# Optimization experiments

Hardware: AMD Instinct MI355X
Metric: run time of the kernel (lower is better)

The kernel has to match this reference:

```python
import jax, jax.numpy as jnp
import numpy as np


def setup_inputs() -> dict:
    key = jax.random.key(0)
    kx, kd = jax.random.split(key)
    B, T, D = 16, 1024, 512
    x = jax.random.normal(kx, (B, T, D), dtype=jnp.float32)
    durations = jax.random.randint(kd, (B, T), 0, 8, dtype=jnp.int64)
    return {"x": x, "durations": durations, "max_len": 4096}


def reference(x, durations, max_len):
    # x: [B,T,D], durations: [B,T] int, max_len: static int
    B, T, D = x.shape
    dur = jnp.maximum(durations.astype(jnp.int32), 0)          # clamp(min=0)
    csum = jnp.cumsum(dur, axis=1)                              # [B,T] inclusive cumsum
    total = csum[:, -1]                                         # [B] total frames per row
    pos = jnp.arange(max_len, dtype=jnp.int32)                  # [L] output frame indices
    # source token for output frame j: first t with csum[t] > j (== repeat_interleave)
    src = jax.vmap(lambda c: jnp.searchsorted(c, pos, side='right'))(csum)  # [B,L]
    src = jnp.minimum(src, T - 1)                               # clamp for out-of-range frames
    out = jnp.take_along_axis(x, src[..., None], axis=1)        # [B,L,D] single parallel gather
    mask = pos[None, :] < total[:, None]                        # [B,L] valid frames
    return jnp.where(mask[..., None], out, jnp.zeros((), x.dtype))
```

## Files before the change

kernel.cpp:

```cpp
#include <hip/hip_runtime.h>


#define BB 16
#define TT 1024
#define DD 512
#define MAXLEN 4096

typedef float v4f __attribute__((ext_vector_type(4)));

__global__ __launch_bounds__(1024) void build_src_kernel(
    const int* __restrict__ dur, int* __restrict__ srcTab) {
  const int b = blockIdx.x;
  const int tid = threadIdx.x;
  const int lane = tid & 63;
  const int wid = tid >> 6;

  const int d = max(dur[b * TT + tid], 0);

  int v = d;
#pragma unroll
  for (int off = 1; off < 64; off <<= 1) {
    int n = __shfl_up(v, off, 64);
    if (lane >= off) v += n;
  }

  __shared__ int wsum[16];
  __shared__ int s_total;
  if (lane == 63) wsum[wid] = v;
  __syncthreads();

  int add = 0;
  for (int i = 0; i < wid; ++i) add += wsum[i];
  const int incl = v + add;
  const int excl = incl - d;

  if (tid == TT - 1) s_total = incl;
  __syncthreads();
  const int total = s_total;

  int* st = srcTab + b * MAXLEN;
  for (int p = excl; p < incl; ++p) st[p] = tid;
  for (int p = total + tid; p < MAXLEN; p += 1024) st[p] = -1;
}

__global__ __launch_bounds__(256) void gather_kernel(
    const v4f* __restrict__ x, const int* __restrict__ srcTab,
    v4f* __restrict__ out) {
  const int gw = (int)(blockIdx.x * 4u + (threadIdx.x >> 6));
  const int lane = threadIdx.x & 63;
  const int base = gw * 4;
  const int b = base >> 12;

  int s[4];
#pragma unroll
  for (int i = 0; i < 4; ++i) s[i] = srcTab[base + i];

  v4f v0[4], v1[4];
  const v4f* xb = x + (size_t)b * TT * (DD / 4);
#pragma unroll
  for (int i = 0; i < 4; ++i) {
    const int src = (s[i] < 0) ? 0 : s[i];
    const v4f* ip = xb + (size_t)src * (DD / 4);
    v0[i] = ip[lane];
    v1[i] = ip[lane + 64];
  }

  const v4f z = {0.f, 0.f, 0.f, 0.f};
#pragma unroll
  for (int i = 0; i < 4; ++i) {
    if (s[i] < 0) { v0[i] = z; v1[i] = z; }
    v4f* op = out + (size_t)(base + i) * (DD / 4);
    __builtin_nontemporal_store(v0[i], op + lane);
    __builtin_nontemporal_store(v1[i], op + lane + 64);
  }
}

extern "C" void kernel_launch(void* const* d_in, const int* in_sizes, int n_in,
                              void* d_out, int out_size, void* d_ws,
                              size_t ws_size, hipStream_t stream) {
  const float* x = (const float*)d_in[0];
  const int* dur = (const int*)d_in[1];
  int* srcTab = (int*)d_ws;

  build_src_kernel<<<BB, 1024, 0, stream>>>(dur, srcTab);

  const int rows = BB * MAXLEN;
  gather_kernel<<<rows / 16, 256, 0, stream>>>((const v4f*)x, srcTab,
                                               (v4f*)d_out);
}
```

Measured before the change: 168.1 us.

## Fuse source-table build into gather kernel with per-block cumsum and binary search

Removes the separate build_src kernel and its global source table. Each gather block now reloads its batch row's durations, recomputes the prefix sum in shared memory, and binary-searches the source token for its 16 output rows. This drops one launch and the serialized 16-block scan kernel. In exchange, the cumsum is recomputed redundantly 256 times per batch row, and two extra block barriers are added before the gather starts.

```diff
diff --git a/kernel.cpp b/kernel.cpp
--- a/kernel.cpp
+++ b/kernel.cpp
@@ -7,71 +7,83 @@
 #define MAXLEN 4096
 
 typedef float v4f __attribute__((ext_vector_type(4)));
+typedef int v4i __attribute__((ext_vector_type(4)));
 
-__global__ __launch_bounds__(1024) void build_src_kernel(
-    const int* __restrict__ dur, int* __restrict__ srcTab) {
-  const int b = blockIdx.x;
+__global__ __launch_bounds__(256) void lr_fused_kernel(
+    const v4f* __restrict__ x, const int* __restrict__ dur,
+    v4f* __restrict__ out) {
+  const int blk = blockIdx.x;
+  const int b = blk >> 8;
+  const int rbase = (blk & 255) << 4;
   const int tid = threadIdx.x;
   const int lane = tid & 63;
   const int wid = tid >> 6;
 
-  const int d = max(dur[b * TT + tid], 0);
+  __shared__ int csum[TT];
+  __shared__ int wsum[4];
+  __shared__ int s_src[16];
 
-  int v = d;
+  const v4i dd = ((const v4i*)(dur + b * TT))[tid];
+  const int d0 = max(dd.x, 0), d1 = max(dd.y, 0);
+  const int d2 = max(dd.z, 0), d3 = max(dd.w, 0);
+  const int l0 = d0, l1 = l0 + d1, l2 = l1 + d2, l3 = l2 + d3;
+
+  int v = l3;
 #pragma unroll
   for (int off = 1; off < 64; off <<= 1) {
-    int n = __shfl_up(v, off, 64);
+    const int n = __shfl_up(v, off, 64);
     if (lane >= off) v += n;
   }
-
-  __shared__ int wsum[16];
-  __shared__ int s_total;
   if (lane == 63) wsum[wid] = v;
   __syncthreads();
 
   int add = 0;
   for (int i = 0; i < wid; ++i) add += wsum[i];
-  const int incl = v + add;
-  const int excl = incl - d;
+  const int total = wsum[0] + wsum[1] + wsum[2] + wsum[3];
+  const int excl = add + v - l3;
+  const int t4 = tid << 2;
+  csum[t4 + 0] = excl + l0;
+  csum[t4 + 1] = excl + l1;
+  csum[t4 + 2] = excl + l2;
+  csum[t4 + 3] = excl + l3;
+  __syncthreads();
 
-  if (tid == TT - 1) s_total = incl;
+  if (tid < 16) {
+    const int pos = rbase + tid;
+    int src = -1;
+    if (pos < total) {
+      int lo = 0, hi = TT;
+      while (lo < hi) {
+        const int mid = (lo + hi) >> 1;
+        if (csum[mid] <= pos) lo = mid + 1;
+        else hi = mid;
+      }
+      src = lo;
+    }
+    s_src[tid] = src;
+  }
   __syncthreads();
-  const int total = s_total;
-
-  int* st = srcTab + b * MAXLEN;
-  for (int p = excl; p < incl; ++p) st[p] = tid;
-  for (int p = total + tid; p < MAXLEN; p += 1024) st[p] = -1;
-}
-
-__global__ __launch_bounds__(256) void gather_kernel(
-    const v4f* __restrict__ x, const int* __restrict__ srcTab,
-    v4f* __restrict__ out) {
-  const int gw = (int)(blockIdx.x * 4u + (threadIdx.x >> 6));
-  const int lane = threadIdx.x & 63;
-  const int base = gw * 4;
-  const int b = base >> 12;
 
   int s[4];
 #pragma unroll
-  for (int i = 0; i < 4; ++i) s[i] = srcTab[base + i];
+  for (int i = 0; i < 4; ++i) s[i] = s_src[wid * 4 + i];
 
-  v4f v0[4], v1[4];
   const v4f* xb = x + (size_t)b * TT * (DD / 4);
+  v4f a0[4], a1[4];
 #pragma unroll
   for (int i = 0; i < 4; ++i) {
     const int src = (s[i] < 0) ? 0 : s[i];
     const v4f* ip = xb + (size_t)src * (DD / 4);
-    v0[i] = ip[lane];
-    v1[i] = ip[lane + 64];
+    a0[i] = ip[lane];
+    a1[i] = ip[lane + 64];
   }
-
   const v4f z = {0.f, 0.f, 0.f, 0.f};
 #pragma unroll
   for (int i = 0; i < 4; ++i) {
-    if (s[i] < 0) { v0[i] = z; v1[i] = z; }
-    v4f* op = out + (size_t)(base + i) * (DD / 4);
-    __builtin_nontemporal_store(v0[i], op + lane);
-    __builtin_nontemporal_store(v1[i], op + lane + 64);
+    if (s[i] < 0) { a0[i] = z; a1[i] = z; }
+    v4f* op = out + (size_t)(b * MAXLEN + rbase + wid * 4 + i) * (DD / 4);
+    __builtin_nontemporal_store(a0[i], op + lane);
+    __builtin_nontemporal_store(a1[i], op + lane + 64);
   }
 }
 
@@ -80,11 +92,8 @@
                               size_t ws_size, hipStream_t stream) {
   const float* x = (const float*)d_in[0];
   const int* dur = (const int*)d_in[1];
-  int* srcTab = (int*)d_ws;
 
-  build_src_kernel<<<BB, 1024, 0, stream>>>(dur, srcTab);
-
-  const int rows = BB * MAXLEN;
-  gather_kernel<<<rows / 16, 256, 0, stream>>>((const v4f*)x, srcTab,
-                                               (v4f*)d_out);
+  const int blocks = BB * (MAXLEN / 16);
+  lr_fused_kernel<<<blocks, 256, 0, stream>>>((const v4f*)x, dur,
+                                              (v4f*)d_out);
 }
```

Result: no change. 165.5 us (-1.6%).
